# Performance work log

Hardware: AMD Instinct MI355X
Metric: run time of the kernel (lower is better)

Reference implementation:

```python
import jax, jax.numpy as jnp
import numpy as np

T, H, I, E, TOP_K = 1024, 1024, 512, 16, 4
SHARED_I = 512  # moe_intermediate_size * n_shared_experts


def setup_inputs() -> dict:
    key = jax.random.key(0)
    ks = jax.random.split(key, 6)
    s = 0.02
    return {
        "hidden_states": jax.random.normal(ks[0], (T, H), dtype=jnp.float32),
        "gate_w": jax.random.normal(ks[1], (E, H), dtype=jnp.float32) * s,          # router weight
        "w_gate_up": jax.random.normal(ks[2], (E, H, 2 * I), dtype=jnp.float32) * s,  # per-expert merged gate/up
        "w_down": jax.random.normal(ks[3], (E, I, H), dtype=jnp.float32) * s,
        "shared_gate_up": jax.random.normal(ks[4], (H, 2 * SHARED_I), dtype=jnp.float32) * s,
        "shared_down": jax.random.normal(ks[5], (SHARED_I, H), dtype=jnp.float32) * s,
    }


def _swiglu(gu):
    g, u = jnp.split(gu, 2, axis=-1)  # gate first, then up (SiluAndMul)
    return jax.nn.silu(g) * u


def reference(hidden_states, gate_w, w_gate_up, w_down, shared_gate_up, shared_down):
    x = hidden_states  # [T, H]
    # ---- router: sigmoid scoring, plain top-k (num_expert_group=topk_group=1), renormalize ----
    logits = x @ gate_w.T                      # [T, E]
    scores = jax.nn.sigmoid(logits)            # [T, E]
    topk_vals, topk_idx = jax.lax.top_k(scores, TOP_K)
    topk_w = topk_vals / jnp.sum(topk_vals, axis=-1, keepdims=True)
    # dense routing matrix [T, E] (zeros for unselected experts)
    route = jnp.zeros_like(scores).at[jnp.arange(T)[:, None], topk_idx].set(topk_w)
    # ---- routed experts: grouped SwiGLU GEMMs, combined by routing weights ----
    gu = jnp.einsum('th,ehf->etf', x, w_gate_up)   # [E, T, 2I]
    h = _swiglu(gu)                                 # [E, T, I]
    eo = jnp.einsum('eti,eih->eth', h, w_down)      # [E, T, H]
    routed = jnp.einsum('te,eth->th', route, eo)    # [T, H]
    # ---- shared expert (routed_scaling_factor = 1.0) ----
    shared = _swiglu(x @ shared_gate_up) @ shared_down  # [T, H]
    return routed + shared
```

## Files before the change

kernel.cpp:

```cpp
#include <hip/hip_runtime.h>
#include <hip/hip_bf16.h>
#include <cstdint>

#define T_TOK 1024
#define H_DIM 1024
#define I_DIM 512
#define E_NUM 16
#define TOPK  4

typedef __bf16 bf16;
typedef __bf16 bf16x4 __attribute__((ext_vector_type(4)));
typedef __bf16 bf16x8 __attribute__((ext_vector_type(8)));
typedef float  f32x4  __attribute__((ext_vector_type(4)));

#define GLOAD16(g, l)                                                                   \
  __builtin_amdgcn_global_load_lds((const __attribute__((address_space(1))) void*)(g),  \
                                   (__attribute__((address_space(3))) void*)(l), 16, 0, 0)

__device__ __forceinline__ unsigned lds_addr(const bf16* p) {
  return (unsigned)(uintptr_t)(const __attribute__((address_space(3))) bf16*)p;
}

template <int OFF>
__device__ __forceinline__ bf16x4 tr_read(unsigned addr) {
  bf16x4 r;
  if constexpr (OFF == 0)
    asm volatile("ds_read_b64_tr_b16 %0, %1" : "=v"(r) : "v"(addr));
  else if constexpr (OFF == 512)
    asm volatile("ds_read_b64_tr_b16 %0, %1 offset:512" : "=v"(r) : "v"(addr));
  else
    asm volatile("ds_read_b64_tr_b16 %0, %1 offset:1024" : "=v"(r) : "v"(addr));
  return r;
}

__device__ __forceinline__ bf16x8 cat8(bf16x4 a, bf16x4 b) {
  return __builtin_shufflevector(a, b, 0, 1, 2, 3, 4, 5, 6, 7);
}

__global__ void prep_kernel(const float* __restrict__ x, bf16* __restrict__ xb,
                            const float* __restrict__ wgu, bf16* __restrict__ wguB,
                            const float* __restrict__ wd, bf16* __restrict__ wdB,
                            const float* __restrict__ sgu, bf16* __restrict__ sguB,
                            const float* __restrict__ sd, bf16* __restrict__ sdB,
                            const float* __restrict__ gw,
                            int* __restrict__ topk_e, float* __restrict__ topk_w,
                            int* __restrict__ counts, int* __restrict__ tok,
                            float* __restrict__ wt, int* __restrict__ slot) {
  const int b = blockIdx.x, tid = threadIdx.x;
  if (b < 1696) {
#pragma unroll
    for (int it = 0; it < 2; ++it) {
      const int task = b + it * 1696;
      const float* src; bf16* dst; int lt;
      if (task < 2048)      { src = wgu; dst = wguB; lt = task; }
      else if (task < 3072) { src = wd;  dst = wdB;  lt = task - 2048; }
      else if (task < 3200) { src = sgu; dst = sguB; lt = task - 3072; }
      else if (task < 3264) { src = sd;  dst = sdB;  lt = task - 3200; }
      else                  { src = x;   dst = xb;   lt = task - 3264; }
      const size_t base = (size_t)lt * 2048 + tid;
      const float4* s4 = (const float4*)src;
      float4 f[8];
#pragma unroll
      for (int q = 0; q < 8; ++q) f[q] = s4[base + (size_t)q * 256];
      bf16x4* d4 = (bf16x4*)dst;
#pragma unroll
      for (int q = 0; q < 8; ++q) {
        bf16x4 p;
        p[0] = (bf16)f[q].x; p[1] = (bf16)f[q].y; p[2] = (bf16)f[q].z; p[3] = (bf16)f[q].w;
        d4[base + (size_t)q * 256] = p;
      }
    }
  } else if (b < 1952) {
    const int wave = tid >> 6, lane = tid & 63;
    const int t = (b - 1696) * 4 + wave;
    const float4* xr = (const float4*)(x + (size_t)t * H_DIM);
    float4 xv[4];
#pragma unroll
    for (int j = 0; j < 4; ++j) xv[j] = xr[lane + 64 * j];
    float p[E_NUM];
#pragma unroll
    for (int e = 0; e < E_NUM; ++e) {
      const float4* gr = (const float4*)(gw + (size_t)e * H_DIM);
      float s = 0.f;
#pragma unroll
      for (int j = 0; j < 4; ++j) {
        float4 g = gr[lane + 64 * j];
        s += xv[j].x * g.x + xv[j].y * g.y + xv[j].z * g.z + xv[j].w * g.w;
      }
      p[e] = s;
    }
#pragma unroll
    for (int off = 32; off > 0; off >>= 1) {
#pragma unroll
      for (int e = 0; e < E_NUM; ++e) p[e] += __shfl_xor(p[e], off);
    }
    float rem[E_NUM];
#pragma unroll
    for (int e = 0; e < E_NUM; ++e) rem[e] = 1.f / (1.f + __expf(-p[e]));
    float vals[TOPK]; int idx[TOPK];
#pragma unroll
    for (int k = 0; k < TOPK; ++k) {
      float m = rem[0]; int mi = 0;
#pragma unroll
      for (int e = 1; e < E_NUM; ++e) {
        if (rem[e] > m) { m = rem[e]; mi = e; }
      }
      vals[k] = m; idx[k] = mi;
#pragma unroll
      for (int e = 0; e < E_NUM; ++e) rem[e] = (e == mi) ? -1e30f : rem[e];
    }
    if (lane == 0) {
      float inv = 1.f / (vals[0] + vals[1] + vals[2] + vals[3]);
      int4 ids; ids.x = idx[0]; ids.y = idx[1]; ids.z = idx[2]; ids.w = idx[3];
      float4 w4; w4.x = vals[0]*inv; w4.y = vals[1]*inv; w4.z = vals[2]*inv; w4.w = vals[3]*inv;
      ((int4*)topk_e)[t] = ids;
      ((float4*)topk_w)[t] = w4;
    }
  } else {
    const int i = (b - 1952) * 256 + tid;
    if (i == 0) counts[E_NUM] = T_TOK;
    tok [E_NUM * T_TOK + i] = i;
    wt  [E_NUM * T_TOK + i] = 1.0f;
    slot[E_NUM * T_TOK + i] = T_TOK * TOPK + i;
  }
}

__global__ void router_build_kernel(const int* __restrict__ topk_e, const float* __restrict__ topk_w,
                                    int* __restrict__ counts, int* __restrict__ tok,
                                    float* __restrict__ wt, int* __restrict__ slot) {
  const int e = blockIdx.x;
  const int tid = threadIdx.x, wave = tid >> 6, lane = tid & 63;
  __shared__ int wsum[4];
  int base = 0;
  for (int r = 0; r < 4; ++r) {
    int t = r * 256 + tid;
    int4 ids = ((const int4*)topk_e)[t];
    int match = -1;
    if (ids.x == e) match = 0;
    if (ids.y == e) match = 1;
    if (ids.z == e) match = 2;
    if (ids.w == e) match = 3;
    unsigned long long bm = __ballot(match >= 0);
    int prefix = __popcll(bm & ((1ull << lane) - 1ull));
    if (lane == 0) wsum[wave] = __popcll(bm);
    __syncthreads();
    int wbase = 0;
#pragma unroll
    for (int wv = 0; wv < 4; ++wv) wbase += (wv < wave) ? wsum[wv] : 0;
    int total = wsum[0] + wsum[1] + wsum[2] + wsum[3];
    if (match >= 0) {
      int pos = base + wbase + prefix;
      tok [e * T_TOK + pos] = t;
      wt  [e * T_TOK + pos] = topk_w[t * 4 + match];
      slot[e * T_TOK + pos] = t * 4 + match;
    }
    base += total;
    __syncthreads();
  }
  if (tid == 0) counts[e] = base;
}

__global__ __launch_bounds__(256, 4)
void gemm1_kernel(const bf16* __restrict__ xb, const bf16* __restrict__ wguB,
                  const bf16* __restrict__ sguB, const int* __restrict__ counts,
                  const int* __restrict__ tok, const float* __restrict__ wt,
                  const int* __restrict__ slot, bf16* __restrict__ hbuf) {
  const int e   = blockIdx.z;
  const int cnt = counts[e];
  const int rt  = blockIdx.y;
  if (rt * 64 >= cnt) return;
  const int nb = blockIdx.x * 64;
  const bf16* WB = (e < E_NUM) ? (wguB + (size_t)e * H_DIM * (2 * I_DIM)) : sguB;

  __shared__ __align__(16) bf16 sA[3][64 * 32];
  __shared__ __align__(16) bf16 sG[3][2048];
  __shared__ __align__(16) bf16 sU[3][2048];

  const int tid = threadIdx.x, wave = tid >> 6, lane = tid & 63;
  const int wr = wave >> 1, wc = wave & 1;
  const int fr = lane & 15, kg = lane >> 4;
  const int lr = lane >> 2, lk = (lane & 3) * 8;

  int ar = rt * 64 + wave * 16 + lr;
  int arc = ar < cnt ? ar : cnt - 1;
  const bf16* aS = xb + (size_t)tok[e * T_TOK + arc] * H_DIM + lk;
  const int aOff = wave * 512;

  const int k_off = 8 * wave + 4 * (lane >> 5) + ((lane & 7) >> 1);
  const int n_off = 16 * ((lane >> 3) & 3) + 8 * (lane & 1);
  const bf16* gS = WB + (size_t)k_off * (2 * I_DIM) + nb + n_off;
  const bf16* uS = WB + (size_t)k_off * (2 * I_DIM) + I_DIM + nb + n_off;
  const int wOff = wave * 512;

  f32x4 accg[2][2], accu[2][2];
#pragma unroll
  for (int i = 0; i < 2; ++i)
#pragma unroll
    for (int j = 0; j < 2; ++j) { accg[i][j] = f32x4{0,0,0,0}; accu[i][j] = f32x4{0,0,0,0}; }

#define STG1(t, bidx) do { size_t ko = (size_t)(t) * 32;    \
    GLOAD16(aS + ko, sA[bidx] + aOff);                      \
    GLOAD16(gS + ko * (2 * I_DIM), sG[bidx] + wOff);        \
    GLOAD16(uS + ko * (2 * I_DIM), sU[bidx] + wOff); } while (0)

  STG1(0, 0); STG1(1, 1);
  const int NT = H_DIM / 32;
  int bufc = 0;
  for (int t = 0; t < NT; ++t) {
    int bn = bufc + 2; bn = bn >= 3 ? bn - 3 : bn;
    if (t + 2 < NT) {
      STG1(t + 2, bn);
      asm volatile("s_waitcnt vmcnt(6)" ::: "memory");
    } else if (t + 1 < NT) {
      asm volatile("s_waitcnt vmcnt(3)" ::: "memory");
    } else {
      asm volatile("s_waitcnt vmcnt(0)" ::: "memory");
    }
    __builtin_amdgcn_s_barrier();
    __builtin_amdgcn_sched_barrier(0);
    const bf16* A = sA[bufc];
    bf16x8 a0 = *(const bf16x8*)(A + (wr * 32      + fr) * 32 + kg * 8);
    bf16x8 a1 = *(const bf16x8*)(A + (wr * 32 + 16 + fr) * 32 + kg * 8);
    unsigned gb = lds_addr(sG[bufc]) + (unsigned)((lane >> 4) << 10) + (unsigned)((lane & 15) << 3);
    unsigned ub = lds_addr(sU[bufc]) + (unsigned)((lane >> 4) << 10) + (unsigned)((lane & 15) << 3);
    unsigned nb0 = (unsigned)(wc * 256), nb1 = nb0 + 128;
    bf16x8 g0 = cat8(tr_read<0>(gb + nb0), tr_read<512>(gb + nb0));
    bf16x8 g1 = cat8(tr_read<0>(gb + nb1), tr_read<512>(gb + nb1));
    bf16x8 u0 = cat8(tr_read<0>(ub + nb0), tr_read<512>(ub + nb0));
    bf16x8 u1 = cat8(tr_read<0>(ub + nb1), tr_read<512>(ub + nb1));
    asm volatile("s_waitcnt lgkmcnt(0)" ::: "memory");
    __builtin_amdgcn_sched_barrier(0);
    accg[0][0] = __builtin_amdgcn_mfma_f32_16x16x32_bf16(a0, g0, accg[0][0], 0, 0, 0);
    accg[0][1] = __builtin_amdgcn_mfma_f32_16x16x32_bf16(a0, g1, accg[0][1], 0, 0, 0);
    accg[1][0] = __builtin_amdgcn_mfma_f32_16x16x32_bf16(a1, g0, accg[1][0], 0, 0, 0);
    accg[1][1] = __builtin_amdgcn_mfma_f32_16x16x32_bf16(a1, g1, accg[1][1], 0, 0, 0);
    accu[0][0] = __builtin_amdgcn_mfma_f32_16x16x32_bf16(a0, u0, accu[0][0], 0, 0, 0);
    accu[0][1] = __builtin_amdgcn_mfma_f32_16x16x32_bf16(a0, u1, accu[0][1], 0, 0, 0);
    accu[1][0] = __builtin_amdgcn_mfma_f32_16x16x32_bf16(a1, u0, accu[1][0], 0, 0, 0);
    accu[1][1] = __builtin_amdgcn_mfma_f32_16x16x32_bf16(a1, u1, accu[1][1], 0, 0, 0);
    __builtin_amdgcn_sched_barrier(0);
    __builtin_amdgcn_s_barrier();
    bufc = bufc == 2 ? 0 : bufc + 1;
  }
#undef STG1

#pragma unroll
  for (int mi = 0; mi < 2; ++mi) {
#pragma unroll
    for (int j = 0; j < 4; ++j) {
      int grow = rt * 64 + wr * 32 + mi * 16 + kg * 4 + j;
      if (grow < cnt) {
        bf16* hr = hbuf + (size_t)slot[e * T_TOK + grow] * I_DIM;
        float w = wt[e * T_TOK + grow];
#pragma unroll
        for (int ni = 0; ni < 2; ++ni) {
          float g = accg[mi][ni][j], u = accu[mi][ni][j];
          float h = w * (g / (1.f + __expf(-g))) * u;
          hr[nb + wc * 32 + ni * 16 + fr] = (bf16)h;
        }
      }
    }
  }
}

__global__ __launch_bounds__(256, 4)
void gemm2_kernel(const bf16* __restrict__ hbuf, const bf16* __restrict__ wdB,
                  const bf16* __restrict__ sdB, const int* __restrict__ counts,
                  const int* __restrict__ slot, float* __restrict__ obuf) {
  const int e   = blockIdx.z;
  const int cnt = counts[e];
  const int rt  = blockIdx.y;
  if (rt * 64 >= cnt) return;
  const int nb = blockIdx.x * 128;
  const bf16* WB = (e < E_NUM) ? (wdB + (size_t)e * I_DIM * H_DIM) : sdB;

  __shared__ __align__(16) bf16 sA[3][64 * 32];
  __shared__ __align__(16) bf16 sB[3][4096];

  const int tid = threadIdx.x, wave = tid >> 6, lane = tid & 63;
  const int wr = wave >> 1, wc = wave & 1;
  const int fr = lane & 15, kg = lane >> 4;
  const int lr = lane >> 2, lk = (lane & 3) * 8;

  int ar = rt * 64 + wave * 16 + lr;
  int arc = ar < cnt ? ar : cnt - 1;
  const bf16* aS = hbuf + (size_t)slot[e * T_TOK + arc] * I_DIM + lk;
  const int aOff = wave * 512;

  const int j2 = (lane & 7) >> 1, h2 = lane & 1, nblk2 = lane >> 3;
  const int n2 = nb + nblk2 * 16 + 8 * h2;
  const bf16* bS0 = WB + (size_t)((wave * 2 + 0) * 4 + j2) * H_DIM + n2;
  const bf16* bS1 = WB + (size_t)((wave * 2 + 1) * 4 + j2) * H_DIM + n2;
  const int bOff0 = wave * 1024;
  const int bOff1 = bOff0 + 512;

  f32x4 acc[2][4];
#pragma unroll
  for (int i = 0; i < 2; ++i)
#pragma unroll
    for (int j = 0; j < 4; ++j) acc[i][j] = f32x4{0,0,0,0};

#define STG2(t, bidx) do { size_t ko = (size_t)(t) * 32;    \
    GLOAD16(aS + ko, sA[bidx] + aOff);                      \
    GLOAD16(bS0 + ko * H_DIM, sB[bidx] + bOff0);            \
    GLOAD16(bS1 + ko * H_DIM, sB[bidx] + bOff1); } while (0)

  STG2(0, 0); STG2(1, 1);
  const int NT = I_DIM / 32;
  int bufc = 0;
  for (int t = 0; t < NT; ++t) {
    int bn = bufc + 2; bn = bn >= 3 ? bn - 3 : bn;
    if (t + 2 < NT) {
      STG2(t + 2, bn);
      asm volatile("s_waitcnt vmcnt(6)" ::: "memory");
    } else if (t + 1 < NT) {
      asm volatile("s_waitcnt vmcnt(3)" ::: "memory");
    } else {
      asm volatile("s_waitcnt vmcnt(0)" ::: "memory");
    }
    __builtin_amdgcn_s_barrier();
    __builtin_amdgcn_sched_barrier(0);
    const bf16* A = sA[bufc];
    bf16x8 a0 = *(const bf16x8*)(A + (wr * 32      + fr) * 32 + kg * 8);
    bf16x8 a1 = *(const bf16x8*)(A + (wr * 32 + 16 + fr) * 32 + kg * 8);
    unsigned bb = lds_addr(sB[bufc]) + (unsigned)((lane >> 4) << 11) + (unsigned)((lane & 15) << 3)
                + (unsigned)(wc * 512);
    bf16x8 b[4];
#pragma unroll
    for (int ni = 0; ni < 4; ++ni)
      b[ni] = cat8(tr_read<0>(bb + ni * 128), tr_read<1024>(bb + ni * 128));
    asm volatile("s_waitcnt lgkmcnt(0)" ::: "memory");
    __builtin_amdgcn_sched_barrier(0);
#pragma unroll
    for (int ni = 0; ni < 4; ++ni) {
      acc[0][ni] = __builtin_amdgcn_mfma_f32_16x16x32_bf16(a0, b[ni], acc[0][ni], 0, 0, 0);
      acc[1][ni] = __builtin_amdgcn_mfma_f32_16x16x32_bf16(a1, b[ni], acc[1][ni], 0, 0, 0);
    }
    __builtin_amdgcn_sched_barrier(0);
    __builtin_amdgcn_s_barrier();
    bufc = bufc == 2 ? 0 : bufc + 1;
  }
#undef STG2

#pragma unroll
  for (int mi = 0; mi < 2; ++mi) {
#pragma unroll
    for (int j = 0; j < 4; ++j) {
      int grow = rt * 64 + wr * 32 + mi * 16 + kg * 4 + j;
      if (grow < cnt) {
        float* orow = obuf + (size_t)slot[e * T_TOK + grow] * H_DIM + nb + wc * 64 + fr;
#pragma unroll
        for (int ni = 0; ni < 4; ++ni)
          orow[ni * 16] = acc[mi][ni][j];
      }
    }
  }
}

__global__ void reduce_kernel(const float* __restrict__ obuf, float* __restrict__ out) {
  const int t = blockIdx.x;
  const int c = threadIdx.x;
  const f32x4* o4 = (const f32x4*)obuf;
  f32x4 s = o4[(size_t)(t * 4 + 0) * 256 + c];
  s += o4[(size_t)(t * 4 + 1) * 256 + c];
  s += o4[(size_t)(t * 4 + 2) * 256 + c];
  s += o4[(size_t)(t * 4 + 3) * 256 + c];
  s += o4[(size_t)(T_TOK * TOPK + t) * 256 + c];
  ((f32x4*)out)[(size_t)t * 256 + c] = s;
}

extern "C" void kernel_launch(void* const* d_in, const int* in_sizes, int n_in,
                              void* d_out, int out_size, void* d_ws, size_t ws_size,
                              hipStream_t stream) {
  const float* x   = (const float*)d_in[0];
  const float* gw  = (const float*)d_in[1];
  const float* wgu = (const float*)d_in[2];
  const float* wd  = (const float*)d_in[3];
  const float* sgu = (const float*)d_in[4];
  const float* sd  = (const float*)d_in[5];
  float* out = (float*)d_out;

  char* ws = (char*)d_ws;
  int*   counts = (int*)  (ws);
  int*   tok    = (int*)  (ws + 1024);
  float* wtA    = (float*)(ws + 70656);
  int*   slotA  = (int*)  (ws + 140288);
  int*   topk_e = (int*)  (ws + 209920);
  float* topk_w = (float*)(ws + 226304);
  bf16*  xb     = (bf16*) (ws + 245760);
  bf16*  hbuf   = (bf16*) (ws + 2342912);
  bf16*  wguB   = (bf16*) (ws + 7585792);
  bf16*  wdB    = (bf16*) (ws + 41140224);
  bf16*  sguB   = (bf16*) (ws + 57917440);
  bf16*  sdB    = (bf16*) (ws + 60014592);
  float* obuf   = (float*)(ws + 7585792);

  prep_kernel<<<1956, 256, 0, stream>>>(x, xb, wgu, wguB, wd, wdB, sgu, sguB, sd, sdB,
                                        gw, topk_e, topk_w, counts, tok, wtA, slotA);
  router_build_kernel<<<E_NUM, 256, 0, stream>>>(topk_e, topk_w, counts, tok, wtA, slotA);
  gemm1_kernel<<<dim3(8, 16, 17), 256, 0, stream>>>(xb, wguB, sguB, counts, tok, wtA, slotA, hbuf);
  gemm2_kernel<<<dim3(8, 16, 17), 256, 0, stream>>>(hbuf, wdB, sdB, counts, slotA, obuf);
  reduce_kernel<<<T_TOK, 256, 0, stream>>>(obuf, out);
}
```

Before: 92.57 us.

## Move down-projection weight conversion from prep kernel into gemm1 grid

Moves the fp32-to-bf16 conversion of the routed and shared down-projection weights out of the prep kernel. It is done instead by extra blocks appended to the gemm1 grid (z slices 17 to 25). Those blocks run alongside the gate/up GEMM blocks, so the memory-bound conversion overlaps with compute and the prep kernel on the critical path gets shorter. The cost is extra blocks competing for CUs with gemm1, and possibly some tail imbalance.

```diff
diff --git a/kernel.cpp b/kernel.cpp
--- a/kernel.cpp
+++ b/kernel.cpp
@@ -37,42 +37,41 @@
   return __builtin_shufflevector(a, b, 0, 1, 2, 3, 4, 5, 6, 7);
 }
 
+__device__ __forceinline__ void conv_task(const float* __restrict__ src,
+                                          bf16* __restrict__ dst, int lt, int tid) {
+  const size_t base = (size_t)lt * 2048 + tid;
+  const float4* s4 = (const float4*)src;
+  float4 f[8];
+#pragma unroll
+  for (int q = 0; q < 8; ++q) f[q] = s4[base + (size_t)q * 256];
+  bf16x4* d4 = (bf16x4*)dst;
+#pragma unroll
+  for (int q = 0; q < 8; ++q) {
+    bf16x4 p;
+    p[0] = (bf16)f[q].x; p[1] = (bf16)f[q].y; p[2] = (bf16)f[q].z; p[3] = (bf16)f[q].w;
+    d4[base + (size_t)q * 256] = p;
+  }
+}
+
 __global__ void prep_kernel(const float* __restrict__ x, bf16* __restrict__ xb,
                             const float* __restrict__ wgu, bf16* __restrict__ wguB,
-                            const float* __restrict__ wd, bf16* __restrict__ wdB,
                             const float* __restrict__ sgu, bf16* __restrict__ sguB,
-                            const float* __restrict__ sd, bf16* __restrict__ sdB,
                             const float* __restrict__ gw,
                             int* __restrict__ topk_e, float* __restrict__ topk_w,
                             int* __restrict__ counts, int* __restrict__ tok,
                             float* __restrict__ wt, int* __restrict__ slot) {
   const int b = blockIdx.x, tid = threadIdx.x;
-  if (b < 1696) {
+  if (b < 1152) {
 #pragma unroll
     for (int it = 0; it < 2; ++it) {
-      const int task = b + it * 1696;
-      const float* src; bf16* dst; int lt;
-      if (task < 2048)      { src = wgu; dst = wguB; lt = task; }
-      else if (task < 3072) { src = wd;  dst = wdB;  lt = task - 2048; }
-      else if (task < 3200) { src = sgu; dst = sguB; lt = task - 3072; }
-      else if (task < 3264) { src = sd;  dst = sdB;  lt = task - 3200; }
-      else                  { src = x;   dst = xb;   lt = task - 3264; }
-      const size_t base = (size_t)lt * 2048 + tid;
-      const float4* s4 = (const float4*)src;
-      float4 f[8];
-#pragma unroll
-      for (int q = 0; q < 8; ++q) f[q] = s4[base + (size_t)q * 256];
-      bf16x4* d4 = (bf16x4*)dst;
-#pragma unroll
-      for (int q = 0; q < 8; ++q) {
-        bf16x4 p;
-        p[0] = (bf16)f[q].x; p[1] = (bf16)f[q].y; p[2] = (bf16)f[q].z; p[3] = (bf16)f[q].w;
-        d4[base + (size_t)q * 256] = p;
-      }
-    }
-  } else if (b < 1952) {
+      const int task = b + it * 1152;
+      if (task < 2048)      conv_task(wgu, wguB, task, tid);
+      else if (task < 2176) conv_task(sgu, sguB, task - 2048, tid);
+      else                  conv_task(x, xb, task - 2176, tid);
+    }
+  } else if (b < 1408) {
     const int wave = tid >> 6, lane = tid & 63;
-    const int t = (b - 1696) * 4 + wave;
+    const int t = (b - 1152) * 4 + wave;
     const float4* xr = (const float4*)(x + (size_t)t * H_DIM);
     float4 xv[4];
 #pragma unroll
@@ -117,7 +116,7 @@
       ((float4*)topk_w)[t] = w4;
     }
   } else {
-    const int i = (b - 1952) * 256 + tid;
+    const int i = (b - 1408) * 256 + tid;
     if (i == 0) counts[E_NUM] = T_TOK;
     tok [E_NUM * T_TOK + i] = i;
     wt  [E_NUM * T_TOK + i] = 1.0f;
@@ -164,8 +163,17 @@
 void gemm1_kernel(const bf16* __restrict__ xb, const bf16* __restrict__ wguB,
                   const bf16* __restrict__ sguB, const int* __restrict__ counts,
                   const int* __restrict__ tok, const float* __restrict__ wt,
-                  const int* __restrict__ slot, bf16* __restrict__ hbuf) {
-  const int e   = blockIdx.z;
+                  const int* __restrict__ slot, bf16* __restrict__ hbuf,
+                  const float* __restrict__ wdF, bf16* __restrict__ wdBo,
+                  const float* __restrict__ sdF, bf16* __restrict__ sdBo) {
+  const int tid = threadIdx.x;
+  const int e = blockIdx.z;
+  if (e >= 17) {
+    const int cid = (e - 17) * 128 + blockIdx.y * 8 + blockIdx.x;
+    if (cid < 1024)      conv_task(wdF, wdBo, cid, tid);
+    else if (cid < 1088) conv_task(sdF, sdBo, cid - 1024, tid);
+    return;
+  }
   const int cnt = counts[e];
   const int rt  = blockIdx.y;
   if (rt * 64 >= cnt) return;
@@ -176,7 +184,7 @@
   __shared__ __align__(16) bf16 sG[3][2048];
   __shared__ __align__(16) bf16 sU[3][2048];
 
-  const int tid = threadIdx.x, wave = tid >> 6, lane = tid & 63;
+  const int wave = tid >> 6, lane = tid & 63;
   const int wr = wave >> 1, wc = wave & 1;
   const int fr = lane & 15, kg = lane >> 4;
   const int lr = lane >> 2, lk = (lane & 3) * 8;
@@ -395,10 +403,11 @@
   bf16*  sdB    = (bf16*) (ws + 60014592);
   float* obuf   = (float*)(ws + 7585792);
 
-  prep_kernel<<<1956, 256, 0, stream>>>(x, xb, wgu, wguB, wd, wdB, sgu, sguB, sd, sdB,
+  prep_kernel<<<1412, 256, 0, stream>>>(x, xb, wgu, wguB, sgu, sguB,
                                         gw, topk_e, topk_w, counts, tok, wtA, slotA);
   router_build_kernel<<<E_NUM, 256, 0, stream>>>(topk_e, topk_w, counts, tok, wtA, slotA);
-  gemm1_kernel<<<dim3(8, 16, 17), 256, 0, stream>>>(xb, wguB, sguB, counts, tok, wtA, slotA, hbuf);
+  gemm1_kernel<<<dim3(8, 16, 26), 256, 0, stream>>>(xb, wguB, sguB, counts, tok, wtA, slotA,
+                                                    hbuf, wd, wdB, sd, sdB);
   gemm2_kernel<<<dim3(8, 16, 17), 256, 0, stream>>>(hbuf, wdB, sdB, counts, slotA, obuf);
   reduce_kernel<<<T_TOK, 256, 0, stream>>>(obuf, out);
 }
```

New measurement: 87.64 us. 5.3% less time.
